# Kernel optimization log

Hardware: AMD Instinct MI355X
Metric: run time of the kernel (lower is better)

Reference implementation:

```python
import jax, jax.numpy as jnp
import numpy as np

P = 4          # number of partitions/devices (hardcoded in the module)
N = 100000     # input nodes per partition
M = 50000      # output (dst) nodes per local graph
E = 400000     # edges per (src,dest) local graph
D = 128        # in_d == out


def _sage_mean(x, W_self, W_neigh, b, src, dst):
    """DGL SAGEConv, aggregator_type='mean', on a bipartite block.
    x: [N, D] src-partition input features (first M rows are dst nodes).
    src/dst: [E] edge endpoints. Returns [M, D]."""
    ones = jnp.ones(src.shape, dtype=x.dtype)
    deg = jax.ops.segment_sum(ones, dst, num_segments=M)            # [M]
    neigh_sum = jax.ops.segment_sum(x[src], dst, num_segments=M)    # [M, D]
    h_neigh = neigh_sum / jnp.maximum(deg, 1.0)[:, None]
    return x[:M] @ W_self + h_neigh @ W_neigh + b


def setup_inputs() -> dict:
    key = jax.random.key(0)
    ks = jax.random.split(key, 6)
    distributed_input = jax.random.normal(ks[0], (P, N, D), dtype=jnp.float32)
    W_self = jax.random.normal(ks[1], (P, D, D), dtype=jnp.float32) / np.sqrt(D)
    W_neigh = jax.random.normal(ks[2], (P, D, D), dtype=jnp.float32) / np.sqrt(D)
    b = jnp.zeros((P, D), dtype=jnp.float32)
    edge_src = jax.random.randint(ks[3], (P, P, E), 0, N, dtype=jnp.int64)
    edge_dst = jax.random.randint(ks[4], (P, P, E), 0, M, dtype=jnp.int64)
    merge_indices = jax.random.randint(ks[5], (P, P, M), 0, M, dtype=jnp.int64)
    return {"distributed_input": distributed_input, "W_self": W_self,
            "W_neigh": W_neigh, "b": b, "edge_src": edge_src,
            "edge_dst": edge_dst, "merge_indices": merge_indices}


def reference(distributed_input, W_self, W_neigh, b, edge_src, edge_dst, merge_indices):
    # Per (src, dest) SAGEConv using src-partition's layer params.
    fp = [[_sage_mean(distributed_input[s], W_self[s], W_neigh[s], b[s],
                      edge_src[s, d], edge_dst[s, d])
           for d in range(P)] for s in range(P)]
    # Cross-partition merge: scatter-add off-diagonal results into diagonal.
    outs = []
    for d in range(P):
        final = fp[d][d]
        for s in range(P):
            if s != d:
                final = final.at[merge_indices[s, d]].add(fp[s][d])
        outs.append(final)
    return jnp.stack(outs)  # [P, M, D]
```

## Files before the change

kernel.cpp:

```cpp
#include <hip/hip_runtime.h>
#include <hip/hip_bf16.h>

#define P 4
#define NN 100000
#define MM 50000
#define EE 400000
#define DD 128
#define ROWS 32

#define SCH 4096
#define NCH 13

typedef __attribute__((ext_vector_type(8))) short bf16x8;
typedef __attribute__((ext_vector_type(4))) float f32x4;

__device__ inline unsigned short bf16u(float x) {
    __hip_bfloat16 h = __float2bfloat16(x);
    return __builtin_bit_cast(unsigned short, h);
}
__device__ inline float bf16f(unsigned short u) {
    return __builtin_bit_cast(float, (unsigned)u << 16);
}

__global__ __launch_bounds__(256) void k_count(const int* __restrict__ edge_dst,
                                               int* __restrict__ deg_orig) {
    int i = blockIdx.x * 256 + threadIdx.x;
    if (i >= P * P * EE) return;
    int pair = i / EE;
    atomicAdd(&deg_orig[pair * MM + edge_dst[i]], 1);
}

__global__ __launch_bounds__(256) void k_derive(const int* __restrict__ merge,
                                                const int* __restrict__ deg_orig,
                                                int* __restrict__ cnt_n,
                                                int* __restrict__ cnt_s) {
    int i = blockIdx.x * 256 + threadIdx.x;
    if (i >= P * P * MM) return;
    int pair = i / MM;
    int r = i - pair * MM;
    int s = pair >> 2, d = pair & 3;
    int m = (s == d) ? r : merge[i];
    atomicAdd(&cnt_n[pair * MM + m], deg_orig[i]);
    atomicAdd(&cnt_s[pair * MM + m], 1);
}

__global__ __launch_bounds__(256) void k_scan1(const int* __restrict__ cnt_n,
                                               const int* __restrict__ cnt_s,
                                               int* __restrict__ partial) {
    int blk = blockIdx.x;
    int chunk = blk % NCH, wp = blk / NCH;
    const int* cnt = ((wp >> 4) ? cnt_s : cnt_n) + (wp & 15) * MM;
    int base = chunk * SCH;
    int end = min(base + SCH, MM);
    int sum = 0;
    for (int i = base + (int)threadIdx.x; i < end; i += 256) sum += cnt[i];
    #pragma unroll
    for (int off = 32; off > 0; off >>= 1) sum += __shfl_down(sum, off);
    __shared__ int sh[4];
    if ((threadIdx.x & 63) == 0) sh[threadIdx.x >> 6] = sum;
    __syncthreads();
    if (threadIdx.x == 0) partial[blk] = sh[0] + sh[1] + sh[2] + sh[3];
}

__global__ __launch_bounds__(256) void k_scan2(int* __restrict__ cnt_n,
                                               int* __restrict__ rs_n,
                                               int* __restrict__ cnt_s,
                                               int* __restrict__ rs_s,
                                               const int* __restrict__ partial) {
    int blk = blockIdx.x;
    int chunk = blk % NCH, wp = blk / NCH;
    int which = wp >> 4, pair = wp & 15;
    int* cnt = (which ? cnt_s : cnt_n) + pair * MM;
    int* rs  = (which ? rs_s : rs_n) + pair * (MM + 1);
    __shared__ int sh[256];
    __shared__ int soff;
    if (threadIdx.x == 0) {
        int o = 0;
        for (int c = 0; c < chunk; ++c) o += partial[wp * NCH + c];
        soff = o;
        if (chunk == NCH - 1) rs[MM] = o + partial[wp * NCH + chunk];
    }
    int base = chunk * SCH + (int)threadIdx.x * 16;
    int v[16]; int run = 0;
    #pragma unroll
    for (int j = 0; j < 16; ++j) {
        int i = base + j;
        int c = (i < MM) ? cnt[i] : 0;
        v[j] = run;
        run += c;
    }
    sh[threadIdx.x] = run;
    __syncthreads();
    for (int off = 1; off < 256; off <<= 1) {
        int t = (threadIdx.x >= (unsigned)off) ? sh[threadIdx.x - off] : 0;
        __syncthreads();
        sh[threadIdx.x] += t;
        __syncthreads();
    }
    int texc = sh[threadIdx.x] - run;
    int o = soff + texc;
    #pragma unroll
    for (int j = 0; j < 16; ++j) {
        int i = base + j;
        if (i < MM) { rs[i] = o + v[j]; cnt[i] = 0; }
    }
}

__global__ __launch_bounds__(256) void k_fill(const int* __restrict__ edge_src,
                                              const int* __restrict__ edge_dst,
                                              const int* __restrict__ merge,
                                              const int* __restrict__ deg_orig,
                                              const int* __restrict__ rs_n,
                                              int* __restrict__ cur_n,
                                              int2* __restrict__ csp) {
    int i = blockIdx.x * 256 + threadIdx.x;
    if (i >= P * P * EE) return;
    int pair = i / EE;
    int s = pair >> 2, d = pair & 3;
    int od = edge_dst[i];
    int m = (s == d) ? od : merge[pair * MM + od];
    float w = 1.0f / fmaxf((float)deg_orig[pair * MM + od], 1.0f);
    int pos = rs_n[pair * (MM + 1) + m] + atomicAdd(&cur_n[pair * MM + m], 1);
    int2 e; e.x = edge_src[i]; e.y = __float_as_int(w);
    csp[(size_t)pair * EE + pos] = e;
}

__global__ __launch_bounds__(256) void k_fill_self(const int* __restrict__ merge,
                                                   const int* __restrict__ rs_s,
                                                   int* __restrict__ cur_s,
                                                   int* __restrict__ css) {
    int i = blockIdx.x * 256 + threadIdx.x;
    if (i >= P * P * MM) return;
    int pair = i / MM;
    int r = i - pair * MM;
    int s = pair >> 2, d = pair & 3;
    int m = (s == d) ? r : merge[i];
    int pos = rs_s[pair * (MM + 1) + m] + atomicAdd(&cur_s[pair * MM + m], 1);
    css[pair * MM + pos] = r;
}

__global__ __launch_bounds__(256) void k_pack_w(const float* __restrict__ Ws,
                                                const float* __restrict__ Wn,
                                                unsigned short* __restrict__ Bpk) {
    int t = blockIdx.x * 256 + threadIdx.x;
    if (t >= 4 * 32 * 128) return;
    int s = t >> 12;
    int rem = t & 4095;
    int c = rem >> 7, col = rem & 127;
    const float* W = (c < 16) ? (Ws + (size_t)s * DD * DD + (c * 8) * DD + col)
                              : (Wn + (size_t)s * DD * DD + ((c - 16) * 8) * DD + col);
    size_t ohi = ((size_t)(s * 2 + 0) * 4096 + rem) * 8;
    size_t olo = ((size_t)(s * 2 + 1) * 4096 + rem) * 8;
    #pragma unroll
    for (int j = 0; j < 8; ++j) {
        float v = W[(size_t)j * DD];
        unsigned short h = bf16u(v);
        unsigned short l = bf16u(v - bf16f(h));
        Bpk[ohi + j] = h;
        Bpk[olo + j] = l;
    }
}

__global__ __launch_bounds__(512, 8) void k_fused(const float* __restrict__ x_all,
                                                  const float* __restrict__ b_all,
                                                  const int* __restrict__ rs_n_all,
                                                  const int2* __restrict__ csp_all,
                                                  const int* __restrict__ rs_s_all,
                                                  const int* __restrict__ css_all,
                                                  const unsigned short* __restrict__ Bpk,
                                                  float* __restrict__ out) {
    int d = blockIdx.y;
    int m0 = blockIdx.x * ROWS;
    int tid = threadIdx.x;
    int lane = tid & 63, wv = tid >> 6;
    int l15 = lane & 15, kg = lane >> 4;

    __shared__ char lds[32768];

    f32x4 acc[2];
    f32x4 zero = {0.f, 0.f, 0.f, 0.f};
    acc[0] = zero; acc[1] = zero;

    for (int s = 0; s < P; ++s) {
        int pair = s * P + d;
        const float* x   = x_all + (size_t)s * NN * DD;
        const int* rsn   = rs_n_all + (size_t)pair * (MM + 1);
        const int2* csp  = csp_all + (size_t)pair * EE;
        const int* rss   = rs_s_all + (size_t)pair * (MM + 1);
        const int* css   = css_all + (size_t)pair * MM;

        for (int r = wv; r < ROWS; r += 8) {
            int m = m0 + r;
            float sx = 0.f, sy = 0.f, nx = 0.f, ny = 0.f;
            if (m < MM) {
                if (s == d) {
                    float2 v = ((const float2*)(x + (size_t)m * DD))[lane];
                    sx = v.x; sy = v.y;
                } else {
                    int e0 = rss[m], e1 = rss[m + 1];
                    for (int e = e0; e < e1; ++e) {
                        float2 v = ((const float2*)(x + (size_t)css[e] * DD))[lane];
                        sx += v.x; sy += v.y;
                    }
                }
                int e0 = rsn[m], e1 = rsn[m + 1];
                int e = e0;
                for (; e + 4 <= e1; e += 4) {
                    int2 c0 = csp[e], c1 = csp[e + 1], c2 = csp[e + 2], c3 = csp[e + 3];
                    float2 v0 = ((const float2*)(x + (size_t)c0.x * DD))[lane];
                    float2 v1 = ((const float2*)(x + (size_t)c1.x * DD))[lane];
                    float2 v2 = ((const float2*)(x + (size_t)c2.x * DD))[lane];
                    float2 v3 = ((const float2*)(x + (size_t)c3.x * DD))[lane];
                    float w0 = __int_as_float(c0.y), w1 = __int_as_float(c1.y);
                    float w2 = __int_as_float(c2.y), w3 = __int_as_float(c3.y);
                    nx += w0 * v0.x + w1 * v1.x + w2 * v2.x + w3 * v3.x;
                    ny += w0 * v0.y + w1 * v1.y + w2 * v2.y + w3 * v3.y;
                }
                for (; e < e1; ++e) {
                    int2 c = csp[e];
                    float w = __int_as_float(c.y);
                    float2 v = ((const float2*)(x + (size_t)c.x * DD))[lane];
                    nx += w * v.x; ny += w * v.y;
                }
            }
            int xr = (r & 7) << 4;
            int rbase = r * 512;
            unsigned short hx = bf16u(sx), hy = bf16u(sy);
            unsigned short lx = bf16u(sx - bf16f(hx)), ly = bf16u(sy - bf16f(hy));
            *(unsigned*)(lds + rbase + ((4 * lane) ^ xr))         = hx | ((unsigned)hy << 16);
            *(unsigned*)(lds + 16384 + rbase + ((4 * lane) ^ xr)) = lx | ((unsigned)ly << 16);
            hx = bf16u(nx); hy = bf16u(ny);
            lx = bf16u(nx - bf16f(hx)); ly = bf16u(ny - bf16f(hy));
            *(unsigned*)(lds + rbase + ((256 + 4 * lane) ^ xr))         = hx | ((unsigned)hy << 16);
            *(unsigned*)(lds + 16384 + rbase + ((256 + 4 * lane) ^ xr)) = lx | ((unsigned)ly << 16);
        }
        __syncthreads();

        {
            int row0 = l15, row1 = 16 + l15;
            int xr = (l15 & 7) << 4;
            const bf16x8* Bh = (const bf16x8*)(Bpk + (size_t)(s * 2 + 0) * 4096 * 8);
            const bf16x8* Bl = (const bf16x8*)(Bpk + (size_t)(s * 2 + 1) * 4096 * 8);
            int colbase = wv * 16 + l15;
            #pragma unroll
            for (int kk = 0; kk < 8; ++kk) {
                int c = kk * 4 + kg;
                int co = (c * 16) ^ xr;
                bf16x8 ah0 = *(const bf16x8*)(lds + row0 * 512 + co);
                bf16x8 ah1 = *(const bf16x8*)(lds + row1 * 512 + co);
                bf16x8 al0 = *(const bf16x8*)(lds + 16384 + row0 * 512 + co);
                bf16x8 al1 = *(const bf16x8*)(lds + 16384 + row1 * 512 + co);
                size_t bo = (size_t)c * 128 + colbase;
                bf16x8 bh = Bh[bo];
                bf16x8 bl = Bl[bo];
                acc[0] = __builtin_amdgcn_mfma_f32_16x16x32_bf16(ah0, bh, acc[0], 0, 0, 0);
                acc[1] = __builtin_amdgcn_mfma_f32_16x16x32_bf16(ah1, bh, acc[1], 0, 0, 0);
                acc[0] = __builtin_amdgcn_mfma_f32_16x16x32_bf16(al0, bh, acc[0], 0, 0, 0);
                acc[1] = __builtin_amdgcn_mfma_f32_16x16x32_bf16(al1, bh, acc[1], 0, 0, 0);
                acc[0] = __builtin_amdgcn_mfma_f32_16x16x32_bf16(ah0, bl, acc[0], 0, 0, 0);
                acc[1] = __builtin_amdgcn_mfma_f32_16x16x32_bf16(ah1, bl, acc[1], 0, 0, 0);
            }
        }

        {
            float bv = b_all[(size_t)s * DD + wv * 16 + l15];
            #pragma unroll
            for (int rt = 0; rt < 2; ++rt) {
                int mb = m0 + rt * 16 + kg * 4;
                #pragma unroll
                for (int r = 0; r < 4; ++r) {
                    int m = mb + r;
                    if (m < MM) {
                        float cf = (float)(rss[m + 1] - rss[m]);
                        acc[rt][r] += cf * bv;
                    }
                }
            }
        }
        __syncthreads();
    }

    float* outd = out + (size_t)d * MM * DD;
    #pragma unroll
    for (int rt = 0; rt < 2; ++rt) {
        #pragma unroll
        for (int r = 0; r < 4; ++r) {
            int m = m0 + rt * 16 + kg * 4 + r;
            if (m >= MM) continue;
            outd[(size_t)m * DD + wv * 16 + l15] = acc[rt][r];
        }
    }
}

extern "C" void kernel_launch(void* const* d_in, const int* in_sizes, int n_in,
                              void* d_out, int out_size, void* d_ws, size_t ws_size,
                              hipStream_t stream) {
    const float* x     = (const float*)d_in[0];
    const float* Ws    = (const float*)d_in[1];
    const float* Wn    = (const float*)d_in[2];
    const float* b     = (const float*)d_in[3];
    const int*   esrc  = (const int*)d_in[4];
    const int*   edst  = (const int*)d_in[5];
    const int*   merge = (const int*)d_in[6];
    float* out = (float*)d_out;

    int* deg_orig = (int*)d_ws;
    int* cnt_n    = deg_orig + 16 * MM;
    int* cnt_s    = cnt_n + 16 * MM;
    int* rs_n     = cnt_s + 16 * MM;
    int* rs_s     = rs_n + 16 * (MM + 1);
    int2* csp     = (int2*)(rs_s + 16 * (MM + 1));
    int* css      = (int*)(csp + (size_t)16 * EE);
    int* partial  = (int*)csp;
    unsigned short* Bpk = (unsigned short*)d_ws;

    hipMemsetAsync(d_ws, 0, sizeof(int) * (size_t)16 * MM * 3, stream);

    int eblocks = (P * P * EE + 255) / 256;
    int mblocks16 = (P * P * MM + 255) / 256;
    k_count<<<eblocks, 256, 0, stream>>>(edst, deg_orig);
    k_derive<<<mblocks16, 256, 0, stream>>>(merge, deg_orig, cnt_n, cnt_s);
    k_scan1<<<2 * 16 * NCH, 256, 0, stream>>>(cnt_n, cnt_s, partial);
    k_scan2<<<2 * 16 * NCH, 256, 0, stream>>>(cnt_n, rs_n, cnt_s, rs_s, partial);
    k_fill<<<eblocks, 256, 0, stream>>>(esrc, edst, merge, deg_orig, rs_n, cnt_n, csp);
    k_fill_self<<<mblocks16, 256, 0, stream>>>(merge, rs_s, cnt_s, css);
    k_pack_w<<<64, 256, 0, stream>>>(Ws, Wn, Bpk);

    dim3 gfused((MM + ROWS - 1) / ROWS, P);
    k_fused<<<gfused, 512, 0, stream>>>(x, b, rs_n, csp, rs_s, css, Bpk, out);
}
```

Measured before the change: 1.774 ms.

## Record atomic ranks during counting and double fused-kernel wave count

The counting and derive kernels now save the per-edge and per-row ranks returned by their atomics into scratch space borrowed from the output buffer. The fill kernels compute positions directly from those ranks, which removes the second pass of contended atomics and the counter re-zeroing in the scan. Separately, the fused kernel launches 1024 threads so that each wave computes one 16x16 output tile instead of two, spreading gather and MFMA work over more waves. The rank8 byte type assumes per-destination degrees below 256. Reusing the output as scratch relies on the fused kernel writing out only after those buffers are no longer read.

Result: faster. 1.721 ms (-3.0%).

```diff
diff --git a/kernel.cpp b/kernel.cpp
--- a/kernel.cpp
+++ b/kernel.cpp
@@ -23,25 +23,29 @@
 }
 
 __global__ __launch_bounds__(256) void k_count(const int* __restrict__ edge_dst,
-                                               int* __restrict__ deg_orig) {
+                                               int* __restrict__ deg_orig,
+                                               unsigned char* __restrict__ rank8) {
     int i = blockIdx.x * 256 + threadIdx.x;
     if (i >= P * P * EE) return;
     int pair = i / EE;
-    atomicAdd(&deg_orig[pair * MM + edge_dst[i]], 1);
+    int r = atomicAdd(&deg_orig[pair * MM + edge_dst[i]], 1);
+    rank8[i] = (unsigned char)r;
 }
 
 __global__ __launch_bounds__(256) void k_derive(const int* __restrict__ merge,
                                                 const int* __restrict__ deg_orig,
                                                 int* __restrict__ cnt_n,
-                                                int* __restrict__ cnt_s) {
+                                                int* __restrict__ cnt_s,
+                                                int* __restrict__ grpoff,
+                                                int* __restrict__ selfrank) {
     int i = blockIdx.x * 256 + threadIdx.x;
     if (i >= P * P * MM) return;
     int pair = i / MM;
     int r = i - pair * MM;
     int s = pair >> 2, d = pair & 3;
     int m = (s == d) ? r : merge[i];
-    atomicAdd(&cnt_n[pair * MM + m], deg_orig[i]);
-    atomicAdd(&cnt_s[pair * MM + m], 1);
+    grpoff[i]   = atomicAdd(&cnt_n[pair * MM + m], deg_orig[i]);
+    selfrank[i] = atomicAdd(&cnt_s[pair * MM + m], 1);
 }
 
 __global__ __launch_bounds__(256) void k_scan1(const int* __restrict__ cnt_n,
@@ -62,15 +66,15 @@
     if (threadIdx.x == 0) partial[blk] = sh[0] + sh[1] + sh[2] + sh[3];
 }
 
-__global__ __launch_bounds__(256) void k_scan2(int* __restrict__ cnt_n,
+__global__ __launch_bounds__(256) void k_scan2(const int* __restrict__ cnt_n,
                                                int* __restrict__ rs_n,
-                                               int* __restrict__ cnt_s,
+                                               const int* __restrict__ cnt_s,
                                                int* __restrict__ rs_s,
                                                const int* __restrict__ partial) {
     int blk = blockIdx.x;
     int chunk = blk % NCH, wp = blk / NCH;
     int which = wp >> 4, pair = wp & 15;
-    int* cnt = (which ? cnt_s : cnt_n) + pair * MM;
+    const int* cnt = (which ? cnt_s : cnt_n) + pair * MM;
     int* rs  = (which ? rs_s : rs_n) + pair * (MM + 1);
     __shared__ int sh[256];
     __shared__ int soff;
@@ -102,7 +106,7 @@
     #pragma unroll
     for (int j = 0; j < 16; ++j) {
         int i = base + j;
-        if (i < MM) { rs[i] = o + v[j]; cnt[i] = 0; }
+        if (i < MM) rs[i] = o + v[j];
     }
 }
 
@@ -111,7 +115,8 @@
                                               const int* __restrict__ merge,
                                               const int* __restrict__ deg_orig,
                                               const int* __restrict__ rs_n,
-                                              int* __restrict__ cur_n,
+                                              const int* __restrict__ grpoff,
+                                              const unsigned char* __restrict__ rank8,
                                               int2* __restrict__ csp) {
     int i = blockIdx.x * 256 + threadIdx.x;
     if (i >= P * P * EE) return;
@@ -120,14 +125,14 @@
     int od = edge_dst[i];
     int m = (s == d) ? od : merge[pair * MM + od];
     float w = 1.0f / fmaxf((float)deg_orig[pair * MM + od], 1.0f);
-    int pos = rs_n[pair * (MM + 1) + m] + atomicAdd(&cur_n[pair * MM + m], 1);
+    int pos = rs_n[pair * (MM + 1) + m] + grpoff[pair * MM + od] + (int)rank8[i];
     int2 e; e.x = edge_src[i]; e.y = __float_as_int(w);
     csp[(size_t)pair * EE + pos] = e;
 }
 
 __global__ __launch_bounds__(256) void k_fill_self(const int* __restrict__ merge,
                                                    const int* __restrict__ rs_s,
-                                                   int* __restrict__ cur_s,
+                                                   const int* __restrict__ selfrank,
                                                    int* __restrict__ css) {
     int i = blockIdx.x * 256 + threadIdx.x;
     if (i >= P * P * MM) return;
@@ -135,7 +140,7 @@
     int r = i - pair * MM;
     int s = pair >> 2, d = pair & 3;
     int m = (s == d) ? r : merge[i];
-    int pos = rs_s[pair * (MM + 1) + m] + atomicAdd(&cur_s[pair * MM + m], 1);
+    int pos = rs_s[pair * (MM + 1) + m] + selfrank[i];
     css[pair * MM + pos] = r;
 }
 
@@ -161,14 +166,14 @@
     }
 }
 
-__global__ __launch_bounds__(512, 8) void k_fused(const float* __restrict__ x_all,
-                                                  const float* __restrict__ b_all,
-                                                  const int* __restrict__ rs_n_all,
-                                                  const int2* __restrict__ csp_all,
-                                                  const int* __restrict__ rs_s_all,
-                                                  const int* __restrict__ css_all,
-                                                  const unsigned short* __restrict__ Bpk,
-                                                  float* __restrict__ out) {
+__global__ __launch_bounds__(1024, 8) void k_fused(const float* __restrict__ x_all,
+                                                   const float* __restrict__ b_all,
+                                                   const int* __restrict__ rs_n_all,
+                                                   const int2* __restrict__ csp_all,
+                                                   const int* __restrict__ rs_s_all,
+                                                   const int* __restrict__ css_all,
+                                                   const unsigned short* __restrict__ Bpk,
+                                                   float* __restrict__ out) {
     int d = blockIdx.y;
     int m0 = blockIdx.x * ROWS;
     int tid = threadIdx.x;
@@ -177,9 +182,11 @@
 
     __shared__ char lds[32768];
 
-    f32x4 acc[2];
-    f32x4 zero = {0.f, 0.f, 0.f, 0.f};
-    acc[0] = zero; acc[1] = zero;
+    f32x4 acc = {0.f, 0.f, 0.f, 0.f};
+
+    int rt = wv & 1;
+    int cp = wv >> 1;
+    int colbase = cp * 16 + l15;
 
     for (int s = 0; s < P; ++s) {
         int pair = s * P + d;
@@ -189,7 +196,7 @@
         const int* rss   = rs_s_all + (size_t)pair * (MM + 1);
         const int* css   = css_all + (size_t)pair * MM;
 
-        for (int r = wv; r < ROWS; r += 8) {
+        for (int r = wv; r < ROWS; r += 16) {
             int m = m0 + r;
             float sx = 0.f, sy = 0.f, nx = 0.f, ny = 0.f;
             if (m < MM) {
@@ -237,43 +244,34 @@
         __syncthreads();
 
         {
-            int row0 = l15, row1 = 16 + l15;
+            int row0 = rt * 16 + l15;
             int xr = (l15 & 7) << 4;
             const bf16x8* Bh = (const bf16x8*)(Bpk + (size_t)(s * 2 + 0) * 4096 * 8);
             const bf16x8* Bl = (const bf16x8*)(Bpk + (size_t)(s * 2 + 1) * 4096 * 8);
-            int colbase = wv * 16 + l15;
             #pragma unroll
             for (int kk = 0; kk < 8; ++kk) {
                 int c = kk * 4 + kg;
                 int co = (c * 16) ^ xr;
-                bf16x8 ah0 = *(const bf16x8*)(lds + row0 * 512 + co);
-                bf16x8 ah1 = *(const bf16x8*)(lds + row1 * 512 + co);
-                bf16x8 al0 = *(const bf16x8*)(lds + 16384 + row0 * 512 + co);
-                bf16x8 al1 = *(const bf16x8*)(lds + 16384 + row1 * 512 + co);
+                bf16x8 ah = *(const bf16x8*)(lds + row0 * 512 + co);
+                bf16x8 al = *(const bf16x8*)(lds + 16384 + row0 * 512 + co);
                 size_t bo = (size_t)c * 128 + colbase;
                 bf16x8 bh = Bh[bo];
                 bf16x8 bl = Bl[bo];
-                acc[0] = __builtin_amdgcn_mfma_f32_16x16x32_bf16(ah0, bh, acc[0], 0, 0, 0);
-                acc[1] = __builtin_amdgcn_mfma_f32_16x16x32_bf16(ah1, bh, acc[1], 0, 0, 0);
-                acc[0] = __builtin_amdgcn_mfma_f32_16x16x32_bf16(al0, bh, acc[0], 0, 0, 0);
-                acc[1] = __builtin_amdgcn_mfma_f32_16x16x32_bf16(al1, bh, acc[1], 0, 0, 0);
-                acc[0] = __builtin_amdgcn_mfma_f32_16x16x32_bf16(ah0, bl, acc[0], 0, 0, 0);
-                acc[1] = __builtin_amdgcn_mfma_f32_16x16x32_bf16(ah1, bl, acc[1], 0, 0, 0);
+                acc = __builtin_amdgcn_mfma_f32_16x16x32_bf16(ah, bh, acc, 0, 0, 0);
+                acc = __builtin_amdgcn_mfma_f32_16x16x32_bf16(al, bh, acc, 0, 0, 0);
+                acc = __builtin_amdgcn_mfma_f32_16x16x32_bf16(ah, bl, acc, 0, 0, 0);
             }
         }
 
         {
-            float bv = b_all[(size_t)s * DD + wv * 16 + l15];
+            float bv = b_all[(size_t)s * DD + colbase];
+            int mb = m0 + rt * 16 + kg * 4;
             #pragma unroll
-            for (int rt = 0; rt < 2; ++rt) {
-                int mb = m0 + rt * 16 + kg * 4;
-                #pragma unroll
-                for (int r = 0; r < 4; ++r) {
-                    int m = mb + r;
-                    if (m < MM) {
-                        float cf = (float)(rss[m + 1] - rss[m]);
-                        acc[rt][r] += cf * bv;
-                    }
+            for (int r = 0; r < 4; ++r) {
+                int m = mb + r;
+                if (m < MM) {
+                    float cf = (float)(rss[m + 1] - rss[m]);
+                    acc[r] += cf * bv;
                 }
             }
         }
@@ -282,13 +280,10 @@
 
     float* outd = out + (size_t)d * MM * DD;
     #pragma unroll
-    for (int rt = 0; rt < 2; ++rt) {
-        #pragma unroll
-        for (int r = 0; r < 4; ++r) {
-            int m = m0 + rt * 16 + kg * 4 + r;
-            if (m >= MM) continue;
-            outd[(size_t)m * DD + wv * 16 + l15] = acc[rt][r];
-        }
+    for (int r = 0; r < 4; ++r) {
+        int m = m0 + rt * 16 + kg * 4 + r;
+        if (m >= MM) continue;
+        outd[(size_t)m * DD + colbase] = acc[r];
     }
 }
 
@@ -314,18 +309,22 @@
     int* partial  = (int*)csp;
     unsigned short* Bpk = (unsigned short*)d_ws;
 
+    int* grpoff   = (int*)out;
+    int* selfrank = grpoff + 16 * MM;
+    unsigned char* rank8 = (unsigned char*)(selfrank + 16 * MM);
+
     hipMemsetAsync(d_ws, 0, sizeof(int) * (size_t)16 * MM * 3, stream);
 
     int eblocks = (P * P * EE + 255) / 256;
     int mblocks16 = (P * P * MM + 255) / 256;
-    k_count<<<eblocks, 256, 0, stream>>>(edst, deg_orig);
-    k_derive<<<mblocks16, 256, 0, stream>>>(merge, deg_orig, cnt_n, cnt_s);
+    k_count<<<eblocks, 256, 0, stream>>>(edst, deg_orig, rank8);
+    k_derive<<<mblocks16, 256, 0, stream>>>(merge, deg_orig, cnt_n, cnt_s, grpoff, selfrank);
     k_scan1<<<2 * 16 * NCH, 256, 0, stream>>>(cnt_n, cnt_s, partial);
     k_scan2<<<2 * 16 * NCH, 256, 0, stream>>>(cnt_n, rs_n, cnt_s, rs_s, partial);
-    k_fill<<<eblocks, 256, 0, stream>>>(esrc, edst, merge, deg_orig, rs_n, cnt_n, csp);
-    k_fill_self<<<mblocks16, 256, 0, stream>>>(merge, rs_s, cnt_s, css);
+    k_fill<<<eblocks, 256, 0, stream>>>(esrc, edst, merge, deg_orig, rs_n, grpoff, rank8, csp);
+    k_fill_self<<<mblocks16, 256, 0, stream>>>(merge, rs_s, selfrank, css);
     k_pack_w<<<64, 256, 0, stream>>>(Ws, Wn, Bpk);
 
     dim3 gfused((MM + ROWS - 1) / ROWS, P);
-    k_fused<<<gfused, 512, 0, stream>>>(x, b, rs_n, csp, rs_s, css, Bpk, out);
-}
+    k_fused<<<gfused, 1024, 0, stream>>>(x, b, rs_n, csp, rs_s, css, Bpk, out);
+}
```

## Record atomic ranks during counting to drop fill-phase atomics; batch gathers

Applied to the files above, without the earlier changes.

The counting kernels now keep the value returned by each atomicAdd: an 8-bit per-edge rank, per-row group offsets and per-row self ranks. A new k_combo kernel precomputes each original row's final CSR base and its mean weight, so k_fill and k_fill_self place entries without atomics or merge lookups. The fused kernel's gather loops are unrolled by 8 (neighbour) and 2 (self), with clamped indices and zero weights for the tail, to keep more loads in flight. The intermediate buffers are placed in the output buffer as scratch, and the 8-bit rank assumes no destination has more than 255 edges.

Result: slower. 1.855 ms (+4.5%).

```diff
diff --git a/kernel.cpp b/kernel.cpp
--- a/kernel.cpp
+++ b/kernel.cpp
@@ -23,25 +23,29 @@
 }
 
 __global__ __launch_bounds__(256) void k_count(const int* __restrict__ edge_dst,
-                                               int* __restrict__ deg_orig) {
+                                               int* __restrict__ deg_orig,
+                                               unsigned char* __restrict__ rank8) {
     int i = blockIdx.x * 256 + threadIdx.x;
     if (i >= P * P * EE) return;
     int pair = i / EE;
-    atomicAdd(&deg_orig[pair * MM + edge_dst[i]], 1);
+    int r = atomicAdd(&deg_orig[pair * MM + edge_dst[i]], 1);
+    rank8[i] = (unsigned char)r;
 }
 
 __global__ __launch_bounds__(256) void k_derive(const int* __restrict__ merge,
                                                 const int* __restrict__ deg_orig,
                                                 int* __restrict__ cnt_n,
-                                                int* __restrict__ cnt_s) {
+                                                int* __restrict__ cnt_s,
+                                                int* __restrict__ grpoff,
+                                                int* __restrict__ selfrank) {
     int i = blockIdx.x * 256 + threadIdx.x;
     if (i >= P * P * MM) return;
     int pair = i / MM;
     int r = i - pair * MM;
     int s = pair >> 2, d = pair & 3;
     int m = (s == d) ? r : merge[i];
-    atomicAdd(&cnt_n[pair * MM + m], deg_orig[i]);
-    atomicAdd(&cnt_s[pair * MM + m], 1);
+    grpoff[i]   = atomicAdd(&cnt_n[pair * MM + m], deg_orig[i]);
+    selfrank[i] = atomicAdd(&cnt_s[pair * MM + m], 1);
 }
 
 __global__ __launch_bounds__(256) void k_scan1(const int* __restrict__ cnt_n,
@@ -62,15 +66,15 @@
     if (threadIdx.x == 0) partial[blk] = sh[0] + sh[1] + sh[2] + sh[3];
 }
 
-__global__ __launch_bounds__(256) void k_scan2(int* __restrict__ cnt_n,
+__global__ __launch_bounds__(256) void k_scan2(const int* __restrict__ cnt_n,
                                                int* __restrict__ rs_n,
-                                               int* __restrict__ cnt_s,
+                                               const int* __restrict__ cnt_s,
                                                int* __restrict__ rs_s,
                                                const int* __restrict__ partial) {
     int blk = blockIdx.x;
     int chunk = blk % NCH, wp = blk / NCH;
     int which = wp >> 4, pair = wp & 15;
-    int* cnt = (which ? cnt_s : cnt_n) + pair * MM;
+    const int* cnt = (which ? cnt_s : cnt_n) + pair * MM;
     int* rs  = (which ? rs_s : rs_n) + pair * (MM + 1);
     __shared__ int sh[256];
     __shared__ int soff;
@@ -102,32 +106,45 @@
     #pragma unroll
     for (int j = 0; j < 16; ++j) {
         int i = base + j;
-        if (i < MM) { rs[i] = o + v[j]; cnt[i] = 0; }
-    }
+        if (i < MM) rs[i] = o + v[j];
+    }
+}
+
+__global__ __launch_bounds__(256) void k_combo(const int* __restrict__ merge,
+                                               const int* __restrict__ deg_orig,
+                                               const int* __restrict__ grpoff,
+                                               const int* __restrict__ rs_n,
+                                               int2* __restrict__ combo) {
+    int i = blockIdx.x * 256 + threadIdx.x;
+    if (i >= P * P * MM) return;
+    int pair = i / MM;
+    int od = i - pair * MM;
+    int s = pair >> 2, d = pair & 3;
+    int m = (s == d) ? od : merge[i];
+    int2 c;
+    c.x = rs_n[pair * (MM + 1) + m] + grpoff[i];
+    c.y = __float_as_int(1.0f / fmaxf((float)deg_orig[i], 1.0f));
+    combo[i] = c;
 }
 
 __global__ __launch_bounds__(256) void k_fill(const int* __restrict__ edge_src,
                                               const int* __restrict__ edge_dst,
-                                              const int* __restrict__ merge,
-                                              const int* __restrict__ deg_orig,
-                                              const int* __restrict__ rs_n,
-                                              int* __restrict__ cur_n,
+                                              const int2* __restrict__ combo,
+                                              const unsigned char* __restrict__ rank8,
                                               int2* __restrict__ csp) {
     int i = blockIdx.x * 256 + threadIdx.x;
     if (i >= P * P * EE) return;
     int pair = i / EE;
-    int s = pair >> 2, d = pair & 3;
     int od = edge_dst[i];
-    int m = (s == d) ? od : merge[pair * MM + od];
-    float w = 1.0f / fmaxf((float)deg_orig[pair * MM + od], 1.0f);
-    int pos = rs_n[pair * (MM + 1) + m] + atomicAdd(&cur_n[pair * MM + m], 1);
-    int2 e; e.x = edge_src[i]; e.y = __float_as_int(w);
+    int2 c = combo[pair * MM + od];
+    int pos = c.x + (int)rank8[i];
+    int2 e; e.x = edge_src[i]; e.y = c.y;
     csp[(size_t)pair * EE + pos] = e;
 }
 
 __global__ __launch_bounds__(256) void k_fill_self(const int* __restrict__ merge,
                                                    const int* __restrict__ rs_s,
-                                                   int* __restrict__ cur_s,
+                                                   const int* __restrict__ selfrank,
                                                    int* __restrict__ css) {
     int i = blockIdx.x * 256 + threadIdx.x;
     if (i >= P * P * MM) return;
@@ -135,7 +152,7 @@
     int r = i - pair * MM;
     int s = pair >> 2, d = pair & 3;
     int m = (s == d) ? r : merge[i];
-    int pos = rs_s[pair * (MM + 1) + m] + atomicAdd(&cur_s[pair * MM + m], 1);
+    int pos = rs_s[pair * (MM + 1) + m] + selfrank[i];
     css[pair * MM + pos] = r;
 }
 
@@ -198,29 +215,33 @@
                     sx = v.x; sy = v.y;
                 } else {
                     int e0 = rss[m], e1 = rss[m + 1];
-                    for (int e = e0; e < e1; ++e) {
-                        float2 v = ((const float2*)(x + (size_t)css[e] * DD))[lane];
-                        sx += v.x; sy += v.y;
+                    int lim = e1 - 1;
+                    for (int eb = e0; eb < e1; eb += 2) {
+                        int i0 = css[min(eb, lim)];
+                        int i1 = css[min(eb + 1, lim)];
+                        float2 v0 = ((const float2*)(x + (size_t)i0 * DD))[lane];
+                        float2 v1 = ((const float2*)(x + (size_t)i1 * DD))[lane];
+                        float w1 = (eb + 1 < e1) ? 1.f : 0.f;
+                        sx += v0.x + w1 * v1.x;
+                        sy += v0.y + w1 * v1.y;
                     }
                 }
                 int e0 = rsn[m], e1 = rsn[m + 1];
-                int e = e0;
-                for (; e + 4 <= e1; e += 4) {
-                    int2 c0 = csp[e], c1 = csp[e + 1], c2 = csp[e + 2], c3 = csp[e + 3];
-                    float2 v0 = ((const float2*)(x + (size_t)c0.x * DD))[lane];
-                    float2 v1 = ((const float2*)(x + (size_t)c1.x * DD))[lane];
-                    float2 v2 = ((const float2*)(x + (size_t)c2.x * DD))[lane];
-                    float2 v3 = ((const float2*)(x + (size_t)c3.x * DD))[lane];
-                    float w0 = __int_as_float(c0.y), w1 = __int_as_float(c1.y);
-                    float w2 = __int_as_float(c2.y), w3 = __int_as_float(c3.y);
-                    nx += w0 * v0.x + w1 * v1.x + w2 * v2.x + w3 * v3.x;
-                    ny += w0 * v0.y + w1 * v1.y + w2 * v2.y + w3 * v3.y;
-                }
-                for (; e < e1; ++e) {
-                    int2 c = csp[e];
-                    float w = __int_as_float(c.y);
-                    float2 v = ((const float2*)(x + (size_t)c.x * DD))[lane];
-                    nx += w * v.x; ny += w * v.y;
+                int lim = e1 - 1;
+                for (int eb = e0; eb < e1; eb += 8) {
+                    int2 c[8];
+                    #pragma unroll
+                    for (int q = 0; q < 8; ++q) c[q] = csp[min(eb + q, lim)];
+                    float2 v[8];
+                    #pragma unroll
+                    for (int q = 0; q < 8; ++q)
+                        v[q] = ((const float2*)(x + (size_t)c[q].x * DD))[lane];
+                    #pragma unroll
+                    for (int q = 0; q < 8; ++q) {
+                        float w = (eb + q < e1) ? __int_as_float(c[q].y) : 0.f;
+                        nx += w * v[q].x;
+                        ny += w * v[q].y;
+                    }
                 }
             }
             int xr = (r & 7) << 4;
@@ -314,16 +335,22 @@
     int* partial  = (int*)csp;
     unsigned short* Bpk = (unsigned short*)d_ws;
 
+    int* grpoff   = (int*)out;
+    int* selfrank = grpoff + 16 * MM;
+    unsigned char* rank8 = (unsigned char*)(selfrank + 16 * MM);
+    int2* combo   = (int2*)(rank8 + (size_t)16 * EE);
+
     hipMemsetAsync(d_ws, 0, sizeof(int) * (size_t)16 * MM * 3, stream);
 
     int eblocks = (P * P * EE + 255) / 256;
     int mblocks16 = (P * P * MM + 255) / 256;
-    k_count<<<eblocks, 256, 0, stream>>>(edst, deg_orig);
-    k_derive<<<mblocks16, 256, 0, stream>>>(merge, deg_orig, cnt_n, cnt_s);
+    k_count<<<eblocks, 256, 0, stream>>>(edst, deg_orig, rank8);
+    k_derive<<<mblocks16, 256, 0, stream>>>(merge, deg_orig, cnt_n, cnt_s, grpoff, selfrank);
     k_scan1<<<2 * 16 * NCH, 256, 0, stream>>>(cnt_n, cnt_s, partial);
     k_scan2<<<2 * 16 * NCH, 256, 0, stream>>>(cnt_n, rs_n, cnt_s, rs_s, partial);
-    k_fill<<<eblocks, 256, 0, stream>>>(esrc, edst, merge, deg_orig, rs_n, cnt_n, csp);
-    k_fill_self<<<mblocks16, 256, 0, stream>>>(merge, rs_s, cnt_s, css);
+    k_combo<<<mblocks16, 256, 0, stream>>>(merge, deg_orig, grpoff, rs_n, combo);
+    k_fill<<<eblocks, 256, 0, stream>>>(esrc, edst, combo, rank8, csp);
+    k_fill_self<<<mblocks16, 256, 0, stream>>>(merge, rs_s, selfrank, css);
     k_pack_w<<<64, 256, 0, stream>>>(Ws, Wn, Bpk);
 
     dim3 gfused((MM + ROWS - 1) / ROWS, P);
```
